# Kernel optimization log

Hardware: AMD Instinct MI355X
Metric: run time of the kernel (lower is better)

The kernel has to match this reference:

```python
import jax, jax.numpy as jnp
import numpy as np
import math

N, M, D, HEADS, RANK = 2048, 512, 256, 8, 32
HD = D // HEADS  # 32
EDGE_P = 0.02


def setup_inputs() -> dict:
    key = jax.random.key(0)
    ks = jax.random.split(key, 12)
    x = jax.random.normal(ks[0], (N, D), jnp.float32)
    # sparse binary incidence matrix; ensure every node is in >=1 hyperedge
    Hinc = (jax.random.uniform(ks[1], (N, M)) < EDGE_P).astype(jnp.float32)
    Hinc = Hinc.at[jnp.arange(N), jnp.arange(N) % M].set(1.0)
    U_r = jax.random.normal(ks[2], (N, RANK), jnp.float32)

    def lin(k, o, i):  # xavier-ish init, torch Linear weight layout [out, in]
        return jax.random.normal(k, (o, i), jnp.float32) * (1.0 / np.sqrt(i)).astype(np.float32)

    return dict(
        x=x, Hinc=Hinc, U_r=U_r,
        Wq=lin(ks[3], D, D), Wk=lin(ks[4], D, D), Wv=lin(ks[5], D, D),
        Wspec=lin(ks[6], D, RANK),
        gn_w=lin(ks[7], HEADS, D), gn_b=jnp.zeros((HEADS,), jnp.float32),
        ge_w=lin(ks[8], HEADS, D), ge_b=jnp.zeros((HEADS,), jnp.float32),
        gs_w=lin(ks[9], HEADS, D), gs_b=jnp.zeros((HEADS,), jnp.float32),
        Wout_w=lin(ks[10], D, D), Wout_b=jnp.zeros((D,), jnp.float32),
        gamma=jnp.ones((D,), jnp.float32), beta=jnp.zeros((D,), jnp.float32),
    )


def reference(x, Hinc, U_r, Wq, Wk, Wv, Wspec, gn_w, gn_b, ge_w, ge_b, gs_w, gs_b, Wout_w, Wout_b, gamma, beta):
    scale = math.sqrt(HD)
    # projections (torch Linear: y = x @ W.T)
    Q = x @ Wq.T
    K = x @ Wk.T
    V = x @ Wv.T
    # node-level masked multi-head attention; mask = (H H^T > 0)
    adj = (Hinc @ Hinc.T) > 0  # [N, N] bool
    Qh = Q.reshape(N, HEADS, HD)
    Kh = K.reshape(N, HEADS, HD)
    Vh = V.reshape(N, HEADS, HD)
    scores = jnp.einsum('nhd,mhd->nhm', Qh, Kh) / scale
    scores = jnp.where(adj[:, None, :], scores, -jnp.inf)
    attn = jax.nn.softmax(scores, axis=-1)
    out_node = jnp.einsum('nhm,mhd->nhd', attn, Vh).reshape(N, D)
    # hyperedge-level attention (unmasked) on aggregated edge features
    h_e = Hinc.T @ x  # [M, D]
    Qe = (h_e @ Wq.T).reshape(M, HEADS, HD)
    Ke = (h_e @ Wk.T).reshape(M, HEADS, HD)
    Ve = (h_e @ Wv.T).reshape(M, HEADS, HD)
    sc = jnp.einsum('mhd,nhd->mhn', Qe, Ke) / scale
    attn_e = jax.nn.softmax(sc, axis=-1)
    h_e_out = jnp.einsum('mhn,nhd->mhd', attn_e, Ve).reshape(M, D)
    out_edge = Hinc @ h_e_out  # scatter edge messages back to nodes
    # spectral branch with sigmoid gate
    spec_feat = U_r @ Wspec.T
    spec_gate = jnp.mean(jax.nn.sigmoid(Q @ gs_w.T + gs_b), axis=-1, keepdims=True)
    out_spec = spec_feat * spec_gate
    # three-way gate normalization
    g_n = jnp.mean(jax.nn.sigmoid(Q @ gn_w.T + gn_b), axis=-1, keepdims=True)
    g_e = jnp.mean(jax.nn.sigmoid(Q @ ge_w.T + ge_b), axis=-1, keepdims=True)
    g_s = jnp.maximum(1.0 - g_n - g_e, 0.0)
    total = g_n + g_e + g_s + 1e-8
    g_n, g_e, g_s = g_n / total, g_e / total, g_s / total
    out = g_n * out_node + g_e * out_edge + g_s * out_spec
    out = out @ Wout_w.T + Wout_b
    # residual (in_dim == out_dim -> residual is x; dropout is identity in eval) + LayerNorm
    y = out + x
    mu = jnp.mean(y, axis=-1, keepdims=True)
    var = jnp.var(y, axis=-1, keepdims=True)
    return gamma * (y - mu) / jnp.sqrt(var + 1e-5) + beta
```

## Files before the change

kernel.cpp:

```cpp
#include <hip/hip_runtime.h>
#include <hip/hip_bf16.h>

#define NN 2048
#define MM 512
#define DIM 256
#define NHEADS 8
#define HD 32
#define RANK 32
#define NSPLIT 4

typedef short bf16x8 __attribute__((ext_vector_type(8)));
typedef float f32x4 __attribute__((ext_vector_type(4)));

__device__ __forceinline__ float sigmoidf(float v) { return 1.f / (1.f + __expf(-v)); }

__device__ __forceinline__ unsigned short f2bf(float f) {
  unsigned u = __float_as_uint(f);
  return (unsigned short)((u + 0x7fffu + ((u >> 16) & 1u)) >> 16);
}
__device__ __forceinline__ float bf2f(unsigned short h) {
  return __uint_as_float(((unsigned)h) << 16);
}

__global__ __launch_bounds__(256) void hilo_multi(
    const float* __restrict__ x, const float* __restrict__ Wq,
    const float* __restrict__ Wk, const float* __restrict__ Wv,
    const float* __restrict__ Wo,
    unsigned short* __restrict__ xh, unsigned short* __restrict__ xl,
    unsigned short* __restrict__ Wqh, unsigned short* __restrict__ Wql,
    unsigned short* __restrict__ Wkh, unsigned short* __restrict__ Wkl,
    unsigned short* __restrict__ Wvh, unsigned short* __restrict__ Wvl,
    unsigned short* __restrict__ Woh, unsigned short* __restrict__ Wol) {
  const int ND = NN * DIM, WSZ = DIM * DIM;
  int i = blockIdx.x * 256 + threadIdx.x;
  const float* src;
  unsigned short *h, *l;
  int off;
  if (i < ND) { src = x; h = xh; l = xl; off = i; }
  else if (i < ND + WSZ) { src = Wq; h = Wqh; l = Wql; off = i - ND; }
  else if (i < ND + 2 * WSZ) { src = Wk; h = Wkh; l = Wkl; off = i - ND - WSZ; }
  else if (i < ND + 3 * WSZ) { src = Wv; h = Wvh; l = Wvl; off = i - ND - 2 * WSZ; }
  else { src = Wo; h = Woh; l = Wol; off = i - ND - 3 * WSZ; }
  float v = src[off];
  unsigned short hh = f2bf(v);
  h[off] = hh;
  l[off] = f2bf(v - bf2f(hh));
}

__global__ __launch_bounds__(256) void build_nodemask(const float* __restrict__ Hinc,
                                                      unsigned long long* __restrict__ nm) {
  int idx = blockIdx.x * blockDim.x + threadIdx.x;
  if (idx >= NN * 8) return;
  int n = idx >> 3, j = idx & 7;
  const float4* src = (const float4*)(Hinc + n * MM + j * 64);
  unsigned long long b = 0ull;
#pragma unroll
  for (int t4 = 0; t4 < 16; ++t4) {
    float4 v = src[t4];
    if (v.x != 0.f) b |= (1ull << (t4 * 4 + 0));
    if (v.y != 0.f) b |= (1ull << (t4 * 4 + 1));
    if (v.z != 0.f) b |= (1ull << (t4 * 4 + 2));
    if (v.w != 0.f) b |= (1ull << (t4 * 4 + 3));
  }
  nm[idx] = b;
}

__global__ __launch_bounds__(64) void transpose_em(const unsigned long long* __restrict__ nm,
                                                   unsigned long long* __restrict__ em) {
  const int rg = blockIdx.x & 31;
  const int cg = blockIdx.x >> 5;
  const int lane = threadIdx.x;
  const unsigned long long w = nm[(size_t)(rg * 64 + lane) * 8 + cg];
  unsigned long long mine = 0ull;
#pragma unroll
  for (int b = 0; b < 64; ++b) {
    unsigned long long res = __ballot((int)((w >> b) & 1ull));
    if (lane == b) mine = res;
  }
  em[(size_t)(cg * 64 + lane) * 32 + rg] = mine;
}

__global__ __launch_bounds__(64) void build_adjbits(const unsigned long long* __restrict__ nm,
                                                    unsigned long long* __restrict__ adjb) {
  __shared__ unsigned long long An[64][8];
  const int nb = blockIdx.x * 64;
  const int mg = blockIdx.y;
  const int lane = threadIdx.x;
#pragma unroll
  for (int j = 0; j < 8; ++j) An[lane][j] = nm[(size_t)(nb + lane) * 8 + j];
  unsigned long long B[8];
#pragma unroll
  for (int j = 0; j < 8; ++j) B[j] = nm[(size_t)(mg * 64 + lane) * 8 + j];
  __syncthreads();
  unsigned long long myw = 0ull;
  for (int nl = 0; nl < 64; ++nl) {
    unsigned long long ov = 0ull;
#pragma unroll
    for (int j = 0; j < 8; ++j) ov |= An[nl][j] & B[j];
    unsigned long long bits = __ballot(ov != 0ull);
    if (lane == nl) myw = bits;
  }
  adjb[(size_t)(nb + lane) * 32 + mg] = myw;
}

__global__ __launch_bounds__(DIM) void edge_aggregate_sparse(const unsigned long long* __restrict__ em,
                                                             const float* __restrict__ x,
                                                             unsigned short* __restrict__ heh,
                                                             unsigned short* __restrict__ hel) {
  int m = blockIdx.x, d = threadIdx.x;
  float acc = 0.f;
  for (int j = 0; j < 32; ++j) {
    unsigned long long b = em[m * 32 + j];
    while (b) {
      int t = __builtin_ctzll(b);
      b &= b - 1;
      acc += x[(j * 64 + t) * DIM + d];
    }
  }
  unsigned short hh = f2bf(acc);
  heh[(size_t)m * DIM + d] = hh;
  hel[(size_t)m * DIM + d] = f2bf(acc - bf2f(hh));
}

__global__ __launch_bounds__(256) void gemm_all_mfma(
    const unsigned short* __restrict__ xh_, const unsigned short* __restrict__ xl_,
    const unsigned short* __restrict__ heh_, const unsigned short* __restrict__ hel_,
    const unsigned short* __restrict__ Wqh_, const unsigned short* __restrict__ Wql_,
    const unsigned short* __restrict__ Wkh_, const unsigned short* __restrict__ Wkl_,
    const unsigned short* __restrict__ Wvh_, const unsigned short* __restrict__ Wvl_,
    unsigned short* __restrict__ Qnh, unsigned short* __restrict__ Qnl,
    unsigned short* __restrict__ Knh, unsigned short* __restrict__ Knl,
    unsigned short* __restrict__ Vnh,
    unsigned short* __restrict__ Qeh, unsigned short* __restrict__ Qel,
    unsigned short* __restrict__ Keh, unsigned short* __restrict__ Kel,
    unsigned short* __restrict__ Veh) {
  const int z = blockIdx.z;
  const bool edge = z >= 3;
  const int zz = edge ? z - 3 : z;
  if (edge && blockIdx.y >= MM / 64) return;
  const int M = edge ? MM : NN;
  const unsigned short* Ahh = edge ? heh_ : xh_;
  const unsigned short* All = edge ? hel_ : xl_;
  const unsigned short* Bh = (zz == 0) ? Wqh_ : (zz == 1) ? Wkh_ : Wvh_;
  const unsigned short* Bl = (zz == 0) ? Wql_ : (zz == 1) ? Wkl_ : Wvl_;
  const float sc = (zz == 0) ? 0.17677669529663687f : 1.f;
  __shared__ uint4 Ah[256], Al[256], Bhs[256], Bls[256];
  const int tid = threadIdx.x;
  const int lane = tid & 63;
  const int wv = tid >> 6, wr = wv >> 1, wc = wv & 1;
  const int g = lane >> 4, c = lane & 15;
  const int y0 = blockIdx.y * 64, o0 = blockIdx.x * 64;
  const int RT = tid >> 6, sg_ = (tid >> 4) & 3, sc_ = tid & 15;
  const int srow = RT * 16 + sc_;
  const int skoff = sg_ * 8;
  f32x4 acc[2][2] = {};
  for (int kc = 0; kc < DIM; kc += 32) {
    __syncthreads();
    Ah[tid] = *(const uint4*)(Ahh + (size_t)(y0 + srow) * DIM + kc + skoff);
    Al[tid] = *(const uint4*)(All + (size_t)(y0 + srow) * DIM + kc + skoff);
    Bhs[tid] = *(const uint4*)(Bh + (size_t)(o0 + srow) * DIM + kc + skoff);
    Bls[tid] = *(const uint4*)(Bl + (size_t)(o0 + srow) * DIM + kc + skoff);
    __syncthreads();
    const bf16x8* Avh = (const bf16x8*)Ah;
    const bf16x8* Avl = (const bf16x8*)Al;
    const bf16x8* Bvh = (const bf16x8*)Bhs;
    const bf16x8* Bvl = (const bf16x8*)Bls;
#pragma unroll
    for (int i = 0; i < 2; ++i)
#pragma unroll
      for (int j = 0; j < 2; ++j) {
        const bf16x8 ah = Avh[(wr * 2 + i) * 64 + lane];
        const bf16x8 al = Avl[(wr * 2 + i) * 64 + lane];
        const bf16x8 bh = Bvh[(wc * 2 + j) * 64 + lane];
        const bf16x8 bl = Bvl[(wc * 2 + j) * 64 + lane];
        acc[i][j] = __builtin_amdgcn_mfma_f32_16x16x32_bf16(ah, bl, acc[i][j], 0, 0, 0);
        acc[i][j] = __builtin_amdgcn_mfma_f32_16x16x32_bf16(al, bh, acc[i][j], 0, 0, 0);
        acc[i][j] = __builtin_amdgcn_mfma_f32_16x16x32_bf16(ah, bh, acc[i][j], 0, 0, 0);
      }
  }
#pragma unroll
  for (int i = 0; i < 2; ++i)
#pragma unroll
    for (int j = 0; j < 2; ++j) {
      const int row = y0 + (wr * 2 + i) * 16 + g * 4;
      const int col = o0 + (wc * 2 + j) * 16 + c;
      if (zz == 2) {
        unsigned short* Vh_g = edge ? Veh : Vnh;
        unsigned short vh[4];
#pragma unroll
        for (int r = 0; r < 4; ++r) vh[r] = f2bf(acc[i][j][r]);
        *(uint2*)(Vh_g + (size_t)col * M + row) =
            make_uint2((unsigned)vh[0] | ((unsigned)vh[1] << 16),
                       (unsigned)vh[2] | ((unsigned)vh[3] << 16));
      } else {
        unsigned short* Ch = (zz == 0) ? (edge ? Qeh : Qnh) : (edge ? Keh : Knh);
        unsigned short* Cl = (zz == 0) ? (edge ? Qel : Qnl) : (edge ? Kel : Knl);
#pragma unroll
        for (int r = 0; r < 4; ++r) {
          float vs = acc[i][j][r] * sc;
          unsigned short hh = f2bf(vs);
          Ch[(size_t)(row + r) * DIM + col] = hh;
          Cl[(size_t)(row + r) * DIM + col] = f2bf(vs - bf2f(hh));
        }
      }
    }
}

__global__ __launch_bounds__(256) void attn_fused(
    const unsigned short* __restrict__ Qnh, const unsigned short* __restrict__ Qnl,
    const unsigned short* __restrict__ Knh, const unsigned short* __restrict__ Knl,
    const unsigned short* __restrict__ Vnh,
    const unsigned int* __restrict__ adjb,
    float* __restrict__ accN, float* __restrict__ lN,
    const unsigned short* __restrict__ Qeh, const unsigned short* __restrict__ Qel,
    const unsigned short* __restrict__ Keh, const unsigned short* __restrict__ Kel,
    const unsigned short* __restrict__ Veh,
    float* __restrict__ accE, float2* __restrict__ mlE) {
  __shared__ uint4 Kfh[2][256], Kfl[2][256], Vfh[2][256];
  __shared__ unsigned short Pq[4][16][72];

  const bool masked = blockIdx.x < (NN / 64);
  const int bx = masked ? blockIdx.x : blockIdx.x - NN / 64;
  const unsigned short* Qh = masked ? Qnh : Qeh;
  const unsigned short* Ql = masked ? Qnl : Qel;
  const unsigned short* Kh = masked ? Knh : Keh;
  const unsigned short* Kl = masked ? Knl : Kel;
  const unsigned short* Vth_g = masked ? Vnh : Veh;
  const int nk = masked ? NN : MM;
  const int nq = nk;

  const int h = blockIdx.y, sp = blockIdx.z;
  const int kspan = nk / NSPLIT;
  const int kbeg = sp * kspan;
  const int kend = kbeg + kspan;
  const int tid = threadIdx.x;
  const int wid = tid >> 6;
  const int lane = tid & 63;
  const int g = lane >> 4, c = lane & 15;
  const int myq = bx * 64 + wid * 16 + c;
  const int nw = nk >> 5;

  const bf16x8 qhi = *(const bf16x8*)(Qh + (size_t)myq * DIM + h * HD + g * 8);
  const bf16x8 qlo = *(const bf16x8*)(Ql + (size_t)myq * DIM + h * HD + g * 8);

  const int sk_key = ((tid >> 6) << 4) | (tid & 15);
  const int sk_g = (tid >> 4) & 3;
  const unsigned short* kh_src = Kh + (size_t)sk_key * DIM + h * HD + sk_g * 8;
  const unsigned short* kl_src = Kl + (size_t)sk_key * DIM + h * HD + sk_g * 8;
  const int sv_rb = tid >> 7, sv_kb = (tid >> 6) & 1;
  const size_t v_row = (size_t)(h * 32 + sv_rb * 16 + (tid & 15)) * nk;
  const int v_off = sv_kb * 32 + ((tid >> 4) & 3) * 8;

  f32x4 acc0 = {0.f, 0.f, 0.f, 0.f}, acc1 = {0.f, 0.f, 0.f, 0.f};
  float l_run = 0.f, m_run = -1e30f;

  uint4 rkh = *(const uint4*)(kh_src + (size_t)kbeg * DIM);
  uint4 rkl = *(const uint4*)(kl_src + (size_t)kbeg * DIM);
  uint4 rvh = *(const uint4*)(Vth_g + v_row + kbeg + v_off);
  Kfh[0][tid] = rkh; Kfl[0][tid] = rkl; Vfh[0][tid] = rvh;
  int cur = 0;

  for (int t = kbeg; t < kend; t += 64) {
    const bool hasNext = (t + 64 < kend);
    if (hasNext) {
      rkh = *(const uint4*)(kh_src + (size_t)(t + 64) * DIM);
      rkl = *(const uint4*)(kl_src + (size_t)(t + 64) * DIM);
      rvh = *(const uint4*)(Vth_g + v_row + (t + 64) + v_off);
    }
    __syncthreads();

    f32x4 s[4];
    const bf16x8* Kfhv = (const bf16x8*)Kfh[cur];
    const bf16x8* Kflv = (const bf16x8*)Kfl[cur];
#pragma unroll
    for (int T = 0; T < 4; ++T) {
      f32x4 z = {0.f, 0.f, 0.f, 0.f};
      f32x4 t1 = __builtin_amdgcn_mfma_f32_16x16x32_bf16(Kfhv[T * 64 + lane], qlo, z, 0, 0, 0);
      t1 = __builtin_amdgcn_mfma_f32_16x16x32_bf16(Kflv[T * 64 + lane], qhi, t1, 0, 0, 0);
      s[T] = __builtin_amdgcn_mfma_f32_16x16x32_bf16(Kfhv[T * 64 + lane], qhi, t1, 0, 0, 0);
    }

    float p[16];
    if (masked) {
      const unsigned w0 = adjb[(size_t)myq * nw + (t >> 5)];
      const unsigned w1 = adjb[(size_t)myq * nw + (t >> 5) + 1];
#pragma unroll
      for (int T = 0; T < 4; ++T) {
        const unsigned w = (T < 2) ? w0 : w1;
#pragma unroll
        for (int r = 0; r < 4; ++r) {
          const int bit = ((T & 1) << 4) + (g << 2) + r;
          const bool valid = (w >> bit) & 1u;
          const float e = valid ? __expf(s[T][r]) : 0.f;
          p[T * 4 + r] = e;
          l_run += e;
        }
      }
    } else {
      float tmax = -1e30f;
#pragma unroll
      for (int T = 0; T < 4; ++T)
#pragma unroll
        for (int r = 0; r < 4; ++r) {
          p[T * 4 + r] = s[T][r];
          tmax = fmaxf(tmax, s[T][r]);
        }
      tmax = fmaxf(tmax, __shfl_xor(tmax, 16));
      tmax = fmaxf(tmax, __shfl_xor(tmax, 32));
      const float mnew = fmaxf(m_run, tmax);
      const float rr = __expf(m_run - mnew);
      float lsum = 0.f;
#pragma unroll
      for (int i = 0; i < 16; ++i) {
        const float e = __expf(p[i] - mnew);
        p[i] = e;
        lsum += e;
      }
      lsum += __shfl_xor(lsum, 16);
      lsum += __shfl_xor(lsum, 32);
      m_run = mnew;
      l_run = l_run * rr + lsum;
#pragma unroll
      for (int r = 0; r < 4; ++r) { acc0[r] *= rr; acc1[r] *= rr; }
    }

#pragma unroll
    for (int T = 0; T < 4; ++T) {
      __hip_bfloat162 b01 = __float22bfloat162_rn(make_float2(p[T * 4 + 0], p[T * 4 + 1]));
      __hip_bfloat162 b23 = __float22bfloat162_rn(make_float2(p[T * 4 + 2], p[T * 4 + 3]));
      unsigned* dst = (unsigned*)&Pq[wid][c][T * 16 + g * 4];
      dst[0] = *(unsigned*)&b01;
      dst[1] = *(unsigned*)&b23;
    }

    const bf16x8* Vh8 = (const bf16x8*)Vfh[cur];
#pragma unroll
    for (int kb = 0; kb < 2; ++kb) {
      const bf16x8 bp = *(const bf16x8*)&Pq[wid][c][kb * 32 + g * 8];
      acc0 = __builtin_amdgcn_mfma_f32_16x16x32_bf16(Vh8[kb * 64 + lane], bp, acc0, 0, 0, 0);
      acc1 = __builtin_amdgcn_mfma_f32_16x16x32_bf16(Vh8[128 + kb * 64 + lane], bp, acc1, 0, 0, 0);
    }

    if (hasNext) {
      const int nb = cur ^ 1;
      Kfh[nb][tid] = rkh; Kfl[nb][tid] = rkl; Vfh[nb][tid] = rvh;
    }
    cur ^= 1;
  }

  if (masked) {
    l_run += __shfl_xor(l_run, 16);
    l_run += __shfl_xor(l_run, 32);
  }

  if (masked) {
    float* pa = accN + ((size_t)sp * nq + myq) * DIM + h * HD;
#pragma unroll
    for (int r = 0; r < 4; ++r) {
      pa[(g << 2) + r] = acc0[r];
      pa[16 + (g << 2) + r] = acc1[r];
    }
    if (g == 0) lN[((size_t)sp * nq + myq) * NHEADS + h] = l_run;
  } else {
    float* pa = accE + ((size_t)sp * nq + myq) * DIM + h * HD;
#pragma unroll
    for (int r = 0; r < 4; ++r) {
      pa[(g << 2) + r] = acc0[r];
      pa[16 + (g << 2) + r] = acc1[r];
    }
    if (g == 0) mlE[((size_t)sp * nq + myq) * NHEADS + h] = make_float2(m_run, l_run);
  }
}

__global__ __launch_bounds__(256) void attn_combine(const float* __restrict__ accS,
                                                    const float2* __restrict__ mlS,
                                                    float* __restrict__ outm,
                                                    int nq, int S) {
  int idx = blockIdx.x * 256 + threadIdx.x;
  int q = idx >> 8;
  int h = (idx >> 5) & 7;
  float M = -1e30f;
  for (int s = 0; s < S; ++s)
    M = fmaxf(M, mlS[((size_t)s * nq + q) * NHEADS + h].x);
  float l = 0.f, o = 0.f;
  for (int s = 0; s < S; ++s) {
    float2 ml = mlS[((size_t)s * nq + q) * NHEADS + h];
    float w = __expf(ml.x - M);
    l += ml.y * w;
    o += accS[((size_t)s * nq + q) * DIM + (idx & 255)] * w;
  }
  outm[idx] = o / l;
}

__global__ __launch_bounds__(64) void gates_kernel(const unsigned short* __restrict__ Qh,
                                                   const unsigned short* __restrict__ Ql,
                                                   const float* __restrict__ gnw, const float* __restrict__ gnb,
                                                   const float* __restrict__ gew, const float* __restrict__ geb,
                                                   const float* __restrict__ gsw, const float* __restrict__ gsb,
                                                   float* __restrict__ gates) {
  int n = blockIdx.x, lane = threadIdx.x;
  const float S = 5.656854249492381f;
  ushort4 qh4 = *(const ushort4*)(Qh + (size_t)n * DIM + lane * 4);
  ushort4 ql4 = *(const ushort4*)(Ql + (size_t)n * DIM + lane * 4);
  float4 q4 = make_float4((bf2f(qh4.x) + bf2f(ql4.x)) * S, (bf2f(qh4.y) + bf2f(ql4.y)) * S,
                          (bf2f(qh4.z) + bf2f(ql4.z)) * S, (bf2f(qh4.w) + bf2f(ql4.w)) * S);
  float accn = 0.f, acce = 0.f, accs = 0.f;
  for (int h = 0; h < NHEADS; ++h) {
    float4 wn = *(const float4*)(gnw + h * DIM + lane * 4);
    float4 we = *(const float4*)(gew + h * DIM + lane * 4);
    float4 ws4 = *(const float4*)(gsw + h * DIM + lane * 4);
    float dn = q4.x * wn.x + q4.y * wn.y + q4.z * wn.z + q4.w * wn.w;
    float de = q4.x * we.x + q4.y * we.y + q4.z * we.z + q4.w * we.w;
    float ds = q4.x * ws4.x + q4.y * ws4.y + q4.z * ws4.z + q4.w * ws4.w;
#pragma unroll
    for (int o = 32; o > 0; o >>= 1) {
      dn += __shfl_xor(dn, o);
      de += __shfl_xor(de, o);
      ds += __shfl_xor(ds, o);
    }
    accn += sigmoidf(dn + gnb[h]);
    acce += sigmoidf(de + geb[h]);
    accs += sigmoidf(ds + gsb[h]);
  }
  if (lane == 0) {
    gates[n * 4 + 0] = accn * 0.125f;
    gates[n * 4 + 1] = acce * 0.125f;
    gates[n * 4 + 2] = accs * 0.125f;
  }
}

__global__ __launch_bounds__(256) void comb_kernel(const float* __restrict__ accS,
                                                   const float* __restrict__ lS,
                                                   const unsigned long long* __restrict__ nm,
                                                   const float* __restrict__ h_e_out,
                                                   const float* __restrict__ gates,
                                                   const float* __restrict__ U_r,
                                                   const float* __restrict__ Wspec,
                                                   unsigned short* __restrict__ Ch,
                                                   unsigned short* __restrict__ Cl) {
  const int n0 = blockIdx.x * 4;
  const int d = threadIdx.x;
  const int h = d >> 5;
  float4 wv[8];
#pragma unroll
  for (int r4 = 0; r4 < 8; ++r4) wv[r4] = *(const float4*)(Wspec + d * RANK + r4 * 4);
#pragma unroll
  for (int nn = 0; nn < 4; ++nn) {
    const int n = n0 + nn;
    float l = 0.f, o = 0.f;
#pragma unroll
    for (int s = 0; s < NSPLIT; ++s) {
      l += lS[((size_t)s * NN + n) * NHEADS + h];
      o += accS[((size_t)s * NN + n) * DIM + d];
    }
    const float onode = o / l;
    float oedge = 0.f;
    for (int j = 0; j < 8; ++j) {
      unsigned long long b = nm[n * 8 + j];
      while (b) {
        int t = __builtin_ctzll(b);
        b &= b - 1;
        oedge += h_e_out[(size_t)(j * 64 + t) * DIM + d];
      }
    }
    float g_n = gates[n * 4 + 0], g_e = gates[n * 4 + 1], sg = gates[n * 4 + 2];
    float g_s = fmaxf(1.f - g_n - g_e, 0.f);
    float tot = g_n + g_e + g_s + 1e-8f;
    g_n /= tot; g_e /= tot; g_s /= tot;
    float spec = 0.f;
#pragma unroll
    for (int r4 = 0; r4 < 8; ++r4) {
      float4 u = *(const float4*)(U_r + n * RANK + r4 * 4);
      spec += u.x * wv[r4].x + u.y * wv[r4].y + u.z * wv[r4].z + u.w * wv[r4].w;
    }
    float cv = g_n * onode + g_e * oedge + g_s * sg * spec;
    unsigned short hh = f2bf(cv);
    Ch[(size_t)n * DIM + d] = hh;
    Cl[(size_t)n * DIM + d] = f2bf(cv - bf2f(hh));
  }
}

__global__ __launch_bounds__(256) void wout_mfma(const unsigned short* __restrict__ Ch,
                                                 const unsigned short* __restrict__ Cl,
                                                 const unsigned short* __restrict__ Wh,
                                                 const unsigned short* __restrict__ Wl,
                                                 const float* __restrict__ x,
                                                 const float* __restrict__ Wout_b,
                                                 float* __restrict__ yws) {
  __shared__ uint4 Ah[256], Al[256], Bh[256], Bl[256];
  const int tid = threadIdx.x;
  const int lane = tid & 63;
  const int wv = tid >> 6;
  const int wr = wv >> 1, wc = wv & 1;
  const int g = lane >> 4, c = lane & 15;
  const int n0 = blockIdx.y * 64, o0 = blockIdx.x * 64;
  const int RT = tid >> 6, sg_ = (tid >> 4) & 3, sc = tid & 15;
  const int srow = RT * 16 + sc;
  const int skoff = sg_ * 8;
  f32x4 acc[2][2] = {};
  for (int kc = 0; kc < DIM; kc += 32) {
    __syncthreads();
    Ah[tid] = *(const uint4*)(Ch + (size_t)(n0 + srow) * DIM + kc + skoff);
    Al[tid] = *(const uint4*)(Cl + (size_t)(n0 + srow) * DIM + kc + skoff);
    Bh[tid] = *(const uint4*)(Wh + (size_t)(o0 + srow) * DIM + kc + skoff);
    Bl[tid] = *(const uint4*)(Wl + (size_t)(o0 + srow) * DIM + kc + skoff);
    __syncthreads();
    const bf16x8* Avh = (const bf16x8*)Ah;
    const bf16x8* Avl = (const bf16x8*)Al;
    const bf16x8* Bvh = (const bf16x8*)Bh;
    const bf16x8* Bvl = (const bf16x8*)Bl;
#pragma unroll
    for (int i = 0; i < 2; ++i)
#pragma unroll
      for (int j = 0; j < 2; ++j) {
        const bf16x8 ah = Avh[(wr * 2 + i) * 64 + lane];
        const bf16x8 al = Avl[(wr * 2 + i) * 64 + lane];
        const bf16x8 bh = Bvh[(wc * 2 + j) * 64 + lane];
        const bf16x8 bl = Bvl[(wc * 2 + j) * 64 + lane];
        acc[i][j] = __builtin_amdgcn_mfma_f32_16x16x32_bf16(ah, bl, acc[i][j], 0, 0, 0);
        acc[i][j] = __builtin_amdgcn_mfma_f32_16x16x32_bf16(al, bh, acc[i][j], 0, 0, 0);
        acc[i][j] = __builtin_amdgcn_mfma_f32_16x16x32_bf16(ah, bh, acc[i][j], 0, 0, 0);
      }
  }
#pragma unroll
  for (int i = 0; i < 2; ++i)
#pragma unroll
    for (int j = 0; j < 2; ++j) {
      const int row = n0 + (wr * 2 + i) * 16 + g * 4;
      const int col = o0 + (wc * 2 + j) * 16 + c;
      const float bias = Wout_b[col];
#pragma unroll
      for (int r = 0; r < 4; ++r)
        yws[(size_t)(row + r) * DIM + col] = acc[i][j][r] + bias + x[(size_t)(row + r) * DIM + col];
    }
}

__global__ __launch_bounds__(DIM) void ln_kernel(const float* __restrict__ yws,
                                                 const float* __restrict__ gamma,
                                                 const float* __restrict__ beta,
                                                 float* __restrict__ out) {
  __shared__ float r1[4], r2[4];
  const int n = blockIdx.x, tid = threadIdx.x;
  const float y = yws[(size_t)n * DIM + tid];
  float s1 = y, s2 = y * y;
#pragma unroll
  for (int o = 32; o > 0; o >>= 1) {
    s1 += __shfl_xor(s1, o);
    s2 += __shfl_xor(s2, o);
  }
  const int wid = tid >> 6, lane = tid & 63;
  if (lane == 0) { r1[wid] = s1; r2[wid] = s2; }
  __syncthreads();
  const float S1 = r1[0] + r1[1] + r1[2] + r1[3];
  const float S2 = r2[0] + r2[1] + r2[2] + r2[3];
  const float mu = S1 * (1.f / DIM);
  const float var = S2 * (1.f / DIM) - mu * mu;
  out[(size_t)n * DIM + tid] = gamma[tid] * (y - mu) * rsqrtf(var + 1e-5f) + beta[tid];
}

extern "C" void kernel_launch(void* const* d_in, const int* in_sizes, int n_in,
                              void* d_out, int out_size, void* d_ws, size_t ws_size,
                              hipStream_t stream) {
  (void)in_sizes; (void)n_in; (void)out_size; (void)ws_size;
  const float* x      = (const float*)d_in[0];
  const float* Hinc   = (const float*)d_in[1];
  const float* U_r    = (const float*)d_in[2];
  const float* Wq     = (const float*)d_in[3];
  const float* Wk     = (const float*)d_in[4];
  const float* Wv     = (const float*)d_in[5];
  const float* Wspec  = (const float*)d_in[6];
  const float* gn_w   = (const float*)d_in[7];
  const float* gn_b   = (const float*)d_in[8];
  const float* ge_w   = (const float*)d_in[9];
  const float* ge_b   = (const float*)d_in[10];
  const float* gs_w   = (const float*)d_in[11];
  const float* gs_b   = (const float*)d_in[12];
  const float* Wout_w = (const float*)d_in[13];
  const float* Wout_b = (const float*)d_in[14];
  const float* gamma  = (const float*)d_in[15];
  const float* beta   = (const float*)d_in[16];
  float* out = (float*)d_out;

  const int ND = NN * DIM;
  const int MD = MM * DIM;
  const int WSZ = DIM * DIM;
  float* ws = (float*)d_ws;
  float* h_e_out  = ws;
  unsigned short* bb = (unsigned short*)(h_e_out + MD);
  unsigned short* xh = bb;
  unsigned short* xl = bb + 1 * (size_t)ND;
  unsigned short* Qbh = bb + 2 * (size_t)ND;
  unsigned short* Qbl = bb + 3 * (size_t)ND;
  unsigned short* Kbh = bb + 4 * (size_t)ND;
  unsigned short* Kbl = bb + 5 * (size_t)ND;
  unsigned short* Vtgh = bb + 6 * (size_t)ND;
  unsigned short* ebb = bb + 7 * (size_t)ND;
  unsigned short* heh = ebb;
  unsigned short* hel = ebb + 1 * (size_t)MD;
  unsigned short* Qeh = ebb + 2 * (size_t)MD;
  unsigned short* Qel = ebb + 3 * (size_t)MD;
  unsigned short* Keh = ebb + 4 * (size_t)MD;
  unsigned short* Kel = ebb + 5 * (size_t)MD;
  unsigned short* Vtgeh = ebb + 6 * (size_t)MD;
  unsigned short* wbb = ebb + 7 * (size_t)MD;
  unsigned short* Wqh = wbb + 0 * WSZ, *Wql = wbb + 1 * WSZ;
  unsigned short* Wkh = wbb + 2 * WSZ, *Wkl = wbb + 3 * WSZ;
  unsigned short* Wvh = wbb + 4 * WSZ, *Wvl = wbb + 5 * WSZ;
  unsigned short* Woh = wbb + 6 * WSZ, *Wol = wbb + 7 * WSZ;
  unsigned long long* nm = (unsigned long long*)(wbb + 8 * WSZ);
  unsigned long long* em = nm + NN * 8;
  unsigned long long* adjb = em + MM * 32;
  float* gates = (float*)(adjb + NN * 32);
  float* accS_n = gates + NN * 4;
  float* lS_n = accS_n + NSPLIT * (size_t)ND;
  float* accS_e = lS_n + NSPLIT * NN * NHEADS;
  float2* mlS_e = (float2*)(accS_e + NSPLIT * (size_t)MD);
  float* yws = accS_e;
  unsigned short* combh = xh;
  unsigned short* combl = xl;

  build_nodemask<<<(NN * 8) / 256, 256, 0, stream>>>(Hinc, nm);
  transpose_em<<<(NN / 64) * (MM / 64), 64, 0, stream>>>(nm, em);
  build_adjbits<<<dim3(NN / 64, 32), 64, 0, stream>>>(nm, adjb);
  hilo_multi<<<(ND + 4 * WSZ) / 256, 256, 0, stream>>>(
      x, Wq, Wk, Wv, Wout_w, xh, xl, Wqh, Wql, Wkh, Wkl, Wvh, Wvl, Woh, Wol);

  edge_aggregate_sparse<<<MM, DIM, 0, stream>>>(em, x, heh, hel);

  gemm_all_mfma<<<dim3(DIM / 64, NN / 64, 6), 256, 0, stream>>>(
      xh, xl, heh, hel, Wqh, Wql, Wkh, Wkl, Wvh, Wvl,
      Qbh, Qbl, Kbh, Kbl, Vtgh,
      Qeh, Qel, Keh, Kel, Vtgeh);

  attn_fused<<<dim3(NN / 64 + MM / 64, NHEADS, NSPLIT), 256, 0, stream>>>(
      Qbh, Qbl, Kbh, Kbl, Vtgh, (const unsigned int*)adjb, accS_n, lS_n,
      Qeh, Qel, Keh, Kel, Vtgeh, accS_e, mlS_e);
  attn_combine<<<(MM * DIM) / 256, 256, 0, stream>>>(accS_e, mlS_e, h_e_out, MM, NSPLIT);

  gates_kernel<<<NN, 64, 0, stream>>>(Qbh, Qbl, gn_w, gn_b, ge_w, ge_b, gs_w, gs_b, gates);

  comb_kernel<<<NN / 4, 256, 0, stream>>>(accS_n, lS_n, nm, h_e_out, gates, U_r, Wspec, combh, combl);
  wout_mfma<<<dim3(DIM / 64, NN / 64), 256, 0, stream>>>(combh, combl, Woh, Wol, x, Wout_b, yws);
  ln_kernel<<<NN, DIM, 0, stream>>>(yws, gamma, beta, out);
}
```

Measured before the change: 121.9 us.

## Merge prep and mask kernels, fuse gates into combine, deepen GEMM K-tile

Node-mask construction moves into the hi/lo bf16 split kernel, and the adjacency-bit and edge-mask transpose kernels become one launch, so three launches go away. The gate computation runs inside the combine kernel, with one wave per node writing to shared memory, which removes a kernel and the global gates buffer. The projection GEMM now stages 64-wide K chunks, halving the number of barrier-separated load phases at the cost of doubling shared memory per block. These cut launch overhead and synchronisation on what is mostly a latency-bound sequence of small kernels.

After: 114.1 us. 6.4% less time.

```diff
diff --git a/kernel.cpp b/kernel.cpp
--- a/kernel.cpp
+++ b/kernel.cpp
@@ -22,7 +22,8 @@
   return __uint_as_float(((unsigned)h) << 16);
 }
 
-__global__ __launch_bounds__(256) void hilo_multi(
+__global__ __launch_bounds__(256) void prep_kernel(
+    const float* __restrict__ Hinc, unsigned long long* __restrict__ nm,
     const float* __restrict__ x, const float* __restrict__ Wq,
     const float* __restrict__ Wk, const float* __restrict__ Wv,
     const float* __restrict__ Wo,
@@ -32,7 +33,23 @@
     unsigned short* __restrict__ Wvh, unsigned short* __restrict__ Wvl,
     unsigned short* __restrict__ Woh, unsigned short* __restrict__ Wol) {
   const int ND = NN * DIM, WSZ = DIM * DIM;
-  int i = blockIdx.x * 256 + threadIdx.x;
+  if (blockIdx.x < 64) {
+    int idx = blockIdx.x * 256 + threadIdx.x;
+    int n = idx >> 3, j = idx & 7;
+    const float4* src = (const float4*)(Hinc + n * MM + j * 64);
+    unsigned long long b = 0ull;
+#pragma unroll
+    for (int t4 = 0; t4 < 16; ++t4) {
+      float4 v = src[t4];
+      if (v.x != 0.f) b |= (1ull << (t4 * 4 + 0));
+      if (v.y != 0.f) b |= (1ull << (t4 * 4 + 1));
+      if (v.z != 0.f) b |= (1ull << (t4 * 4 + 2));
+      if (v.w != 0.f) b |= (1ull << (t4 * 4 + 3));
+    }
+    nm[idx] = b;
+    return;
+  }
+  int i = (blockIdx.x - 64) * 256 + threadIdx.x;
   const float* src;
   unsigned short *h, *l;
   int off;
@@ -47,60 +64,42 @@
   l[off] = f2bf(v - bf2f(hh));
 }
 
-__global__ __launch_bounds__(256) void build_nodemask(const float* __restrict__ Hinc,
-                                                      unsigned long long* __restrict__ nm) {
-  int idx = blockIdx.x * blockDim.x + threadIdx.x;
-  if (idx >= NN * 8) return;
-  int n = idx >> 3, j = idx & 7;
-  const float4* src = (const float4*)(Hinc + n * MM + j * 64);
-  unsigned long long b = 0ull;
-#pragma unroll
-  for (int t4 = 0; t4 < 16; ++t4) {
-    float4 v = src[t4];
-    if (v.x != 0.f) b |= (1ull << (t4 * 4 + 0));
-    if (v.y != 0.f) b |= (1ull << (t4 * 4 + 1));
-    if (v.z != 0.f) b |= (1ull << (t4 * 4 + 2));
-    if (v.w != 0.f) b |= (1ull << (t4 * 4 + 3));
-  }
-  nm[idx] = b;
-}
-
-__global__ __launch_bounds__(64) void transpose_em(const unsigned long long* __restrict__ nm,
-                                                   unsigned long long* __restrict__ em) {
-  const int rg = blockIdx.x & 31;
-  const int cg = blockIdx.x >> 5;
+__global__ __launch_bounds__(64) void mask_derive(const unsigned long long* __restrict__ nm,
+                                                  unsigned long long* __restrict__ adjb,
+                                                  unsigned long long* __restrict__ em) {
   const int lane = threadIdx.x;
-  const unsigned long long w = nm[(size_t)(rg * 64 + lane) * 8 + cg];
-  unsigned long long mine = 0ull;
-#pragma unroll
-  for (int b = 0; b < 64; ++b) {
-    unsigned long long res = __ballot((int)((w >> b) & 1ull));
-    if (lane == b) mine = res;
-  }
-  em[(size_t)(cg * 64 + lane) * 32 + rg] = mine;
-}
-
-__global__ __launch_bounds__(64) void build_adjbits(const unsigned long long* __restrict__ nm,
-                                                    unsigned long long* __restrict__ adjb) {
-  __shared__ unsigned long long An[64][8];
-  const int nb = blockIdx.x * 64;
-  const int mg = blockIdx.y;
-  const int lane = threadIdx.x;
-#pragma unroll
-  for (int j = 0; j < 8; ++j) An[lane][j] = nm[(size_t)(nb + lane) * 8 + j];
-  unsigned long long B[8];
-#pragma unroll
-  for (int j = 0; j < 8; ++j) B[j] = nm[(size_t)(mg * 64 + lane) * 8 + j];
-  __syncthreads();
-  unsigned long long myw = 0ull;
-  for (int nl = 0; nl < 64; ++nl) {
-    unsigned long long ov = 0ull;
-#pragma unroll
-    for (int j = 0; j < 8; ++j) ov |= An[nl][j] & B[j];
-    unsigned long long bits = __ballot(ov != 0ull);
-    if (lane == nl) myw = bits;
-  }
-  adjb[(size_t)(nb + lane) * 32 + mg] = myw;
+  if (blockIdx.x < 1024) {
+    __shared__ unsigned long long An[64][8];
+    const int nb = (blockIdx.x >> 5) * 64;
+    const int mg = blockIdx.x & 31;
+#pragma unroll
+    for (int j = 0; j < 8; ++j) An[lane][j] = nm[(size_t)(nb + lane) * 8 + j];
+    unsigned long long B[8];
+#pragma unroll
+    for (int j = 0; j < 8; ++j) B[j] = nm[(size_t)(mg * 64 + lane) * 8 + j];
+    __syncthreads();
+    unsigned long long myw = 0ull;
+    for (int nl = 0; nl < 64; ++nl) {
+      unsigned long long ov = 0ull;
+#pragma unroll
+      for (int j = 0; j < 8; ++j) ov |= An[nl][j] & B[j];
+      unsigned long long bits = __ballot(ov != 0ull);
+      if (lane == nl) myw = bits;
+    }
+    adjb[(size_t)(nb + lane) * 32 + mg] = myw;
+  } else {
+    const int bid = blockIdx.x - 1024;
+    const int rg = bid & 31;
+    const int cg = bid >> 5;
+    const unsigned long long w = nm[(size_t)(rg * 64 + lane) * 8 + cg];
+    unsigned long long mine = 0ull;
+#pragma unroll
+    for (int b = 0; b < 64; ++b) {
+      unsigned long long res = __ballot((int)((w >> b) & 1ull));
+      if (lane == b) mine = res;
+    }
+    em[(size_t)(cg * 64 + lane) * 32 + rg] = mine;
+  }
 }
 
 __global__ __launch_bounds__(DIM) void edge_aggregate_sparse(const unsigned long long* __restrict__ em,
@@ -144,7 +143,7 @@
   const unsigned short* Bh = (zz == 0) ? Wqh_ : (zz == 1) ? Wkh_ : Wvh_;
   const unsigned short* Bl = (zz == 0) ? Wql_ : (zz == 1) ? Wkl_ : Wvl_;
   const float sc = (zz == 0) ? 0.17677669529663687f : 1.f;
-  __shared__ uint4 Ah[256], Al[256], Bhs[256], Bls[256];
+  __shared__ uint4 Ah[512], Al[512], Bhs[512], Bls[512];
   const int tid = threadIdx.x;
   const int lane = tid & 63;
   const int wv = tid >> 6, wr = wv >> 1, wc = wv & 1;
@@ -154,29 +153,37 @@
   const int srow = RT * 16 + sc_;
   const int skoff = sg_ * 8;
   f32x4 acc[2][2] = {};
-  for (int kc = 0; kc < DIM; kc += 32) {
+  for (int kc = 0; kc < DIM; kc += 64) {
     __syncthreads();
     Ah[tid] = *(const uint4*)(Ahh + (size_t)(y0 + srow) * DIM + kc + skoff);
+    Ah[256 + tid] = *(const uint4*)(Ahh + (size_t)(y0 + srow) * DIM + kc + 32 + skoff);
     Al[tid] = *(const uint4*)(All + (size_t)(y0 + srow) * DIM + kc + skoff);
+    Al[256 + tid] = *(const uint4*)(All + (size_t)(y0 + srow) * DIM + kc + 32 + skoff);
     Bhs[tid] = *(const uint4*)(Bh + (size_t)(o0 + srow) * DIM + kc + skoff);
+    Bhs[256 + tid] = *(const uint4*)(Bh + (size_t)(o0 + srow) * DIM + kc + 32 + skoff);
     Bls[tid] = *(const uint4*)(Bl + (size_t)(o0 + srow) * DIM + kc + skoff);
+    Bls[256 + tid] = *(const uint4*)(Bl + (size_t)(o0 + srow) * DIM + kc + 32 + skoff);
     __syncthreads();
     const bf16x8* Avh = (const bf16x8*)Ah;
     const bf16x8* Avl = (const bf16x8*)Al;
     const bf16x8* Bvh = (const bf16x8*)Bhs;
     const bf16x8* Bvl = (const bf16x8*)Bls;
 #pragma unroll
-    for (int i = 0; i < 2; ++i)
-#pragma unroll
-      for (int j = 0; j < 2; ++j) {
-        const bf16x8 ah = Avh[(wr * 2 + i) * 64 + lane];
-        const bf16x8 al = Avl[(wr * 2 + i) * 64 + lane];
-        const bf16x8 bh = Bvh[(wc * 2 + j) * 64 + lane];
-        const bf16x8 bl = Bvl[(wc * 2 + j) * 64 + lane];
-        acc[i][j] = __builtin_amdgcn_mfma_f32_16x16x32_bf16(ah, bl, acc[i][j], 0, 0, 0);
-        acc[i][j] = __builtin_amdgcn_mfma_f32_16x16x32_bf16(al, bh, acc[i][j], 0, 0, 0);
-        acc[i][j] = __builtin_amdgcn_mfma_f32_16x16x32_bf16(ah, bh, acc[i][j], 0, 0, 0);
-      }
+    for (int ks = 0; ks < 2; ++ks) {
+      const int kb = ks * 256;
+#pragma unroll
+      for (int i = 0; i < 2; ++i)
+#pragma unroll
+        for (int j = 0; j < 2; ++j) {
+          const bf16x8 ah = Avh[kb + (wr * 2 + i) * 64 + lane];
+          const bf16x8 al = Avl[kb + (wr * 2 + i) * 64 + lane];
+          const bf16x8 bh = Bvh[kb + (wc * 2 + j) * 64 + lane];
+          const bf16x8 bl = Bvl[kb + (wc * 2 + j) * 64 + lane];
+          acc[i][j] = __builtin_amdgcn_mfma_f32_16x16x32_bf16(ah, bl, acc[i][j], 0, 0, 0);
+          acc[i][j] = __builtin_amdgcn_mfma_f32_16x16x32_bf16(al, bh, acc[i][j], 0, 0, 0);
+          acc[i][j] = __builtin_amdgcn_mfma_f32_16x16x32_bf16(ah, bh, acc[i][j], 0, 0, 0);
+        }
+    }
   }
 #pragma unroll
   for (int i = 0; i < 2; ++i)
@@ -392,54 +399,58 @@
   outm[idx] = o / l;
 }
 
-__global__ __launch_bounds__(64) void gates_kernel(const unsigned short* __restrict__ Qh,
+__global__ __launch_bounds__(256) void comb_kernel(const float* __restrict__ accS,
+                                                   const float* __restrict__ lS,
+                                                   const unsigned long long* __restrict__ nm,
+                                                   const float* __restrict__ h_e_out,
+                                                   const unsigned short* __restrict__ Qh,
                                                    const unsigned short* __restrict__ Ql,
                                                    const float* __restrict__ gnw, const float* __restrict__ gnb,
                                                    const float* __restrict__ gew, const float* __restrict__ geb,
                                                    const float* __restrict__ gsw, const float* __restrict__ gsb,
-                                                   float* __restrict__ gates) {
-  int n = blockIdx.x, lane = threadIdx.x;
-  const float S = 5.656854249492381f;
-  ushort4 qh4 = *(const ushort4*)(Qh + (size_t)n * DIM + lane * 4);
-  ushort4 ql4 = *(const ushort4*)(Ql + (size_t)n * DIM + lane * 4);
-  float4 q4 = make_float4((bf2f(qh4.x) + bf2f(ql4.x)) * S, (bf2f(qh4.y) + bf2f(ql4.y)) * S,
-                          (bf2f(qh4.z) + bf2f(ql4.z)) * S, (bf2f(qh4.w) + bf2f(ql4.w)) * S);
-  float accn = 0.f, acce = 0.f, accs = 0.f;
-  for (int h = 0; h < NHEADS; ++h) {
-    float4 wn = *(const float4*)(gnw + h * DIM + lane * 4);
-    float4 we = *(const float4*)(gew + h * DIM + lane * 4);
-    float4 ws4 = *(const float4*)(gsw + h * DIM + lane * 4);
-    float dn = q4.x * wn.x + q4.y * wn.y + q4.z * wn.z + q4.w * wn.w;
-    float de = q4.x * we.x + q4.y * we.y + q4.z * we.z + q4.w * we.w;
-    float ds = q4.x * ws4.x + q4.y * ws4.y + q4.z * ws4.z + q4.w * ws4.w;
-#pragma unroll
-    for (int o = 32; o > 0; o >>= 1) {
-      dn += __shfl_xor(dn, o);
-      de += __shfl_xor(de, o);
-      ds += __shfl_xor(ds, o);
-    }
-    accn += sigmoidf(dn + gnb[h]);
-    acce += sigmoidf(de + geb[h]);
-    accs += sigmoidf(ds + gsb[h]);
-  }
-  if (lane == 0) {
-    gates[n * 4 + 0] = accn * 0.125f;
-    gates[n * 4 + 1] = acce * 0.125f;
-    gates[n * 4 + 2] = accs * 0.125f;
-  }
-}
-
-__global__ __launch_bounds__(256) void comb_kernel(const float* __restrict__ accS,
-                                                   const float* __restrict__ lS,
-                                                   const unsigned long long* __restrict__ nm,
-                                                   const float* __restrict__ h_e_out,
-                                                   const float* __restrict__ gates,
                                                    const float* __restrict__ U_r,
                                                    const float* __restrict__ Wspec,
                                                    unsigned short* __restrict__ Ch,
                                                    unsigned short* __restrict__ Cl) {
+  __shared__ float gl[4][3];
   const int n0 = blockIdx.x * 4;
-  const int d = threadIdx.x;
+  const int tid = threadIdx.x;
+  const int w = tid >> 6, lane = tid & 63;
+
+  {
+    const int n = n0 + w;
+    const float S = 5.656854249492381f;
+    ushort4 qh4 = *(const ushort4*)(Qh + (size_t)n * DIM + lane * 4);
+    ushort4 ql4 = *(const ushort4*)(Ql + (size_t)n * DIM + lane * 4);
+    float4 q4 = make_float4((bf2f(qh4.x) + bf2f(ql4.x)) * S, (bf2f(qh4.y) + bf2f(ql4.y)) * S,
+                            (bf2f(qh4.z) + bf2f(ql4.z)) * S, (bf2f(qh4.w) + bf2f(ql4.w)) * S);
+    float accn = 0.f, acce = 0.f, accs = 0.f;
+    for (int h = 0; h < NHEADS; ++h) {
+      float4 wn = *(const float4*)(gnw + h * DIM + lane * 4);
+      float4 we = *(const float4*)(gew + h * DIM + lane * 4);
+      float4 ws4 = *(const float4*)(gsw + h * DIM + lane * 4);
+      float dn = q4.x * wn.x + q4.y * wn.y + q4.z * wn.z + q4.w * wn.w;
+      float de = q4.x * we.x + q4.y * we.y + q4.z * we.z + q4.w * we.w;
+      float ds = q4.x * ws4.x + q4.y * ws4.y + q4.z * ws4.z + q4.w * ws4.w;
+#pragma unroll
+      for (int o = 32; o > 0; o >>= 1) {
+        dn += __shfl_xor(dn, o);
+        de += __shfl_xor(de, o);
+        ds += __shfl_xor(ds, o);
+      }
+      accn += sigmoidf(dn + gnb[h]);
+      acce += sigmoidf(de + geb[h]);
+      accs += sigmoidf(ds + gsb[h]);
+    }
+    if (lane == 0) {
+      gl[w][0] = accn * 0.125f;
+      gl[w][1] = acce * 0.125f;
+      gl[w][2] = accs * 0.125f;
+    }
+  }
+  __syncthreads();
+
+  const int d = tid;
   const int h = d >> 5;
   float4 wv[8];
 #pragma unroll
@@ -463,7 +474,7 @@
         oedge += h_e_out[(size_t)(j * 64 + t) * DIM + d];
       }
     }
-    float g_n = gates[n * 4 + 0], g_e = gates[n * 4 + 1], sg = gates[n * 4 + 2];
+    float g_n = gl[nn][0], g_e = gl[nn][1], sg = gl[nn][2];
     float g_s = fmaxf(1.f - g_n - g_e, 0.f);
     float tot = g_n + g_e + g_s + 1e-8f;
     g_n /= tot; g_e /= tot; g_s /= tot;
@@ -610,8 +621,7 @@
   unsigned long long* nm = (unsigned long long*)(wbb + 8 * WSZ);
   unsigned long long* em = nm + NN * 8;
   unsigned long long* adjb = em + MM * 32;
-  float* gates = (float*)(adjb + NN * 32);
-  float* accS_n = gates + NN * 4;
+  float* accS_n = (float*)(adjb + NN * 32);
   float* lS_n = accS_n + NSPLIT * (size_t)ND;
   float* accS_e = lS_n + NSPLIT * NN * NHEADS;
   float2* mlS_e = (float2*)(accS_e + NSPLIT * (size_t)MD);
@@ -619,11 +629,10 @@
   unsigned short* combh = xh;
   unsigned short* combl = xl;
 
-  build_nodemask<<<(NN * 8) / 256, 256, 0, stream>>>(Hinc, nm);
-  transpose_em<<<(NN / 64) * (MM / 64), 64, 0, stream>>>(nm, em);
-  build_adjbits<<<dim3(NN / 64, 32), 64, 0, stream>>>(nm, adjb);
-  hilo_multi<<<(ND + 4 * WSZ) / 256, 256, 0, stream>>>(
-      x, Wq, Wk, Wv, Wout_w, xh, xl, Wqh, Wql, Wkh, Wkl, Wvh, Wvl, Woh, Wol);
+  prep_kernel<<<64 + (ND + 4 * WSZ) / 256, 256, 0, stream>>>(
+      Hinc, nm, x, Wq, Wk, Wv, Wout_w,
+      xh, xl, Wqh, Wql, Wkh, Wkl, Wvh, Wvl, Woh, Wol);
+  mask_derive<<<2048, 64, 0, stream>>>(nm, adjb, em);
 
   edge_aggregate_sparse<<<MM, DIM, 0, stream>>>(em, x, heh, hel);
 
@@ -637,9 +646,9 @@
       Qeh, Qel, Keh, Kel, Vtgeh, accS_e, mlS_e);
   attn_combine<<<(MM * DIM) / 256, 256, 0, stream>>>(accS_e, mlS_e, h_e_out, MM, NSPLIT);
 
-  gates_kernel<<<NN, 64, 0, stream>>>(Qbh, Qbl, gn_w, gn_b, ge_w, ge_b, gs_w, gs_b, gates);
-
-  comb_kernel<<<NN / 4, 256, 0, stream>>>(accS_n, lS_n, nm, h_e_out, gates, U_r, Wspec, combh, combl);
+  comb_kernel<<<NN / 4, 256, 0, stream>>>(accS_n, lS_n, nm, h_e_out, Qbh, Qbl,
+                                          gn_w, gn_b, ge_w, ge_b, gs_w, gs_b,
+                                          U_r, Wspec, combh, combl);
   wout_mfma<<<dim3(DIM / 64, NN / 64), 256, 0, stream>>>(combh, combl, Woh, Wol, x, Wout_b, yws);
   ln_kernel<<<NN, DIM, 0, stream>>>(yws, gamma, beta, out);
 }
```
